# Kernel tuning notes

Hardware: AMD Instinct MI355X
Metric: run time of the kernel (lower is better)

## Reference

```python
import jax, jax.numpy as jnp
import numpy as np

B, I, O = 2048, 512, 512

def setup_inputs() -> dict:
    key = jax.random.key(0)
    kx, kw, ks = jax.random.split(key, 3)
    x = jax.random.uniform(kx, (B, I), dtype=jnp.float32)
    # shift weight logits so sigmoid(w) ~ 0.02: keeps the length-I product
    # of implication factors away from underflow (sparse conjunction)
    w_logits = jax.random.normal(kw, (I, O), dtype=jnp.float32) - 4.0
    s_logits = jax.random.normal(ks, (I, O), dtype=jnp.float32)
    return {"x": x, "w_logits": w_logits, "s_logits": s_logits}

def reference(x, w_logits, s_logits):
    # FuzzyParam.value(): sigmoid of stored logits
    w = jax.nn.sigmoid(w_logits)   # (I, O)
    s = jax.nn.sigmoid(s_logits)   # (I, O)
    xi = x[:, :, None]             # (B, I, 1)
    # product fuzzy logic:
    #   bin_xnor(a, b) = a*b + (1-a)*(1-b)
    #   implies(a, b)  = 1 - a*(1 - b)
    #   conjoin        = prod along axis
    xnor = xi * s + (1.0 - xi) * (1.0 - s)      # (B, I, O)
    factors = 1.0 - w * (1.0 - xnor)            # (B, I, O)
    return jnp.prod(factors, axis=1)            # (B, O)
```

## Files before the change

### kernel.cpp

```cpp
#include <hip/hip_runtime.h>
#include <math.h>

#define B_DIM 2048
#define I_DIM 512
#define O_DIM 512

constexpr int LANES = 64;
constexpr int T_O   = 4;
constexpr int O_BLK = LANES * T_O;
constexpr int NW    = 8;
constexpr int R_BLK = 8;
constexpr int QPC   = (I_DIM / 4) / NW;

__global__ __launch_bounds__(256) void setup_kernel(
    const float* __restrict__ w_logits,
    const float* __restrict__ s_logits,
    float4* __restrict__ ab4)
{
    int t  = blockIdx.x * 256 + threadIdx.x;
    int o  = t & (O_DIM - 1);
    int k  = t >> 9;
    int i0 = 2 * k;

    float zw0 = w_logits[(i0 + 0) * O_DIM + o];
    float zs0 = s_logits[(i0 + 0) * O_DIM + o];
    float zw1 = w_logits[(i0 + 1) * O_DIM + o];
    float zs1 = s_logits[(i0 + 1) * O_DIM + o];

    float w0 = 1.0f / (1.0f + expf(-zw0));
    float s0 = 1.0f / (1.0f + expf(-zs0));
    float w1 = 1.0f / (1.0f + expf(-zw1));
    float s1 = 1.0f / (1.0f + expf(-zs1));

    float4 v;
    v.x = fmaf(-w0, s0, 1.0f);
    v.y = fmaf(-w1, s1, 1.0f);
    v.z = w0 * (2.0f * s0 - 1.0f);
    v.w = w1 * (2.0f * s1 - 1.0f);
    ab4[k * O_DIM + o] = v;
}

__global__ __launch_bounds__(512, 2) void fuzzy_main(
    const float* __restrict__ x,
    const float4* __restrict__ ab4,
    float* __restrict__ out)
{
    __shared__ __align__(16) unsigned char sh_raw[64 * 1024];
    float (*part)[R_BLK][O_BLK] =
        reinterpret_cast<float(*)[R_BLK][O_BLK]>(sh_raw);

    const int lane  = threadIdx.x;
    const int y     = __builtin_amdgcn_readfirstlane((int)threadIdx.y);
    const int tid   = y * LANES + lane;
    const int bid   = blockIdx.x;
    const int obase = (bid & 1) * O_BLK;
    const int b0    = (bid >> 1) * R_BLK;
    const int qbase = y * QPC;

    const float* xb = x + (size_t)b0 * I_DIM + qbase * 4;

    const float4* abp = ab4 + obase + lane;

    float4 cA0[T_O], cA1[T_O], cB0[T_O], cB1[T_O];
#pragma unroll
    for (int j = 0; j < T_O; ++j) {
        cA0[j] = abp[(size_t)(2 * qbase + 0) * O_DIM + 64 * j];
        cA1[j] = abp[(size_t)(2 * qbase + 1) * O_DIM + 64 * j];
        cB0[j] = abp[(size_t)(2 * qbase + 2) * O_DIM + 64 * j];
        cB1[j] = abp[(size_t)(2 * qbase + 3) * O_DIM + 64 * j];
    }

    float acc[R_BLK][T_O];
#pragma unroll
    for (int r = 0; r < R_BLK; ++r)
#pragma unroll
        for (int j = 0; j < T_O; ++j) acc[r][j] = 1.0f;

#pragma unroll 1
    for (int qq = 0; qq < QPC; qq += 2) {
        float4 xqA[R_BLK], xqB[R_BLK];
#pragma unroll
        for (int r = 0; r < R_BLK; ++r) {
            const float* xr = xb + r * I_DIM + qq * 4;
            xqA[r] = *(const float4*)(xr);
            xqB[r] = *(const float4*)(xr + 4);
        }
        {
            const int q = qbase + qq;
            float4 nA0[T_O], nA1[T_O];
#pragma unroll
            for (int j = 0; j < T_O; ++j) {
                nA0[j] = abp[(size_t)(2 * q + 4) * O_DIM + 64 * j];
                nA1[j] = abp[(size_t)(2 * q + 5) * O_DIM + 64 * j];
            }
#pragma unroll
            for (int r = 0; r < R_BLK; ++r) {
#pragma unroll
                for (int j = 0; j < T_O; ++j) {
                    float f0 = fmaf(cA0[j].z, xqA[r].x, cA0[j].x);
                    float f1 = fmaf(cA0[j].w, xqA[r].y, cA0[j].y);
                    float f2 = fmaf(cA1[j].z, xqA[r].z, cA1[j].x);
                    float f3 = fmaf(cA1[j].w, xqA[r].w, cA1[j].y);
                    acc[r][j] *= (f0 * f2) * (f1 * f3);
                }
            }
#pragma unroll
            for (int j = 0; j < T_O; ++j) { cA0[j] = nA0[j]; cA1[j] = nA1[j]; }
        }
        {
            const int q = qbase + qq + 1;
            float4 nB0[T_O], nB1[T_O];
#pragma unroll
            for (int j = 0; j < T_O; ++j) {
                nB0[j] = abp[(size_t)(2 * q + 4) * O_DIM + 64 * j];
                nB1[j] = abp[(size_t)(2 * q + 5) * O_DIM + 64 * j];
            }
#pragma unroll
            for (int r = 0; r < R_BLK; ++r) {
#pragma unroll
                for (int j = 0; j < T_O; ++j) {
                    float f0 = fmaf(cB0[j].z, xqB[r].x, cB0[j].x);
                    float f1 = fmaf(cB0[j].w, xqB[r].y, cB0[j].y);
                    float f2 = fmaf(cB1[j].z, xqB[r].z, cB1[j].x);
                    float f3 = fmaf(cB1[j].w, xqB[r].w, cB1[j].y);
                    acc[r][j] *= (f0 * f2) * (f1 * f3);
                }
            }
#pragma unroll
            for (int j = 0; j < T_O; ++j) { cB0[j] = nB0[j]; cB1[j] = nB1[j]; }
        }
    }

    if (y < 4) {
#pragma unroll
        for (int r = 0; r < R_BLK; ++r)
#pragma unroll
            for (int j = 0; j < T_O; ++j)
                part[y][r][64 * j + lane] = acc[r][j];
    }
    __syncthreads();
    if (y >= 4) {
#pragma unroll
        for (int r = 0; r < R_BLK; ++r)
#pragma unroll
            for (int j = 0; j < T_O; ++j)
                part[y - 4][r][64 * j + lane] *= acc[r][j];
    }
    __syncthreads();
#pragma unroll
    for (int p = 0; p < 4; ++p) {
        int idx = p * 512 + tid;
        int r = idx >> 8;
        int c = idx & (O_BLK - 1);
        float v = part[0][r][c] * part[1][r][c]
                * part[2][r][c] * part[3][r][c];
        out[(size_t)(b0 + r) * O_DIM + obase + c] = v;
    }
}

extern "C" void kernel_launch(void* const* d_in, const int* in_sizes, int n_in,
                              void* d_out, int out_size, void* d_ws, size_t ws_size,
                              hipStream_t stream) {
    const float* x        = (const float*)d_in[0];
    const float* w_logits = (const float*)d_in[1];
    const float* s_logits = (const float*)d_in[2];
    float* out = (float*)d_out;
    float4* ab4 = (float4*)d_ws;

    setup_kernel<<<dim3(512), dim3(256), 0, stream>>>(w_logits, s_logits, ab4);

    fuzzy_main<<<dim3(512), dim3(LANES, NW), 0, stream>>>(
        x, ab4, out);
}
```

Measured before the change: 89.53 us.

## Factor out per-column constant product so inner loop uses one FMA per term

Rewrites each factor a+b*x as a*(1+(b/a)*x). The product of the a terms over I is precomputed per output column in two small setup kernels and applied once at the end. The main loop now loads one float4 of ratios per four inputs instead of two, which halves coefficient traffic and register use while keeping the same FMA and multiply count. It adds an extra single-block kernel launch and relies on a being nonzero and the product not underflowing, which can shift numerical rounding.

```diff
diff --git a/kernel.cpp b/kernel.cpp
--- a/kernel.cpp
+++ b/kernel.cpp
@@ -12,37 +12,57 @@
 constexpr int R_BLK = 8;
 constexpr int QPC   = (I_DIM / 4) / NW;
 
-__global__ __launch_bounds__(256) void setup_kernel(
+#define APROD_OFF (1u << 20)
+#define PO_OFF    ((1u << 20) + (1u << 18))
+
+__global__ __launch_bounds__(256) void setup_c(
     const float* __restrict__ w_logits,
     const float* __restrict__ s_logits,
-    float4* __restrict__ ab4)
+    float4* __restrict__ cT,
+    float*  __restrict__ aprod)
 {
-    int t  = blockIdx.x * 256 + threadIdx.x;
-    int o  = t & (O_DIM - 1);
-    int k  = t >> 9;
-    int i0 = 2 * k;
+    int t = blockIdx.x * 256 + threadIdx.x;
+    int o = t & (O_DIM - 1);
+    int q = t >> 9;
 
-    float zw0 = w_logits[(i0 + 0) * O_DIM + o];
-    float zs0 = s_logits[(i0 + 0) * O_DIM + o];
-    float zw1 = w_logits[(i0 + 1) * O_DIM + o];
-    float zs1 = s_logits[(i0 + 1) * O_DIM + o];
+    float c[4], pa = 1.0f;
+#pragma unroll
+    for (int u = 0; u < 4; ++u) {
+        int i = 4 * q + u;
+        float zw = w_logits[(size_t)i * O_DIM + o];
+        float zs = s_logits[(size_t)i * O_DIM + o];
+        float w = 1.0f / (1.0f + expf(-zw));
+        float s = 1.0f / (1.0f + expf(-zs));
+        float a = fmaf(-w, s, 1.0f);
+        float b = w * (2.0f * s - 1.0f);
+        c[u] = b / a;
+        pa *= a;
+    }
+    float4 v; v.x = c[0]; v.y = c[1]; v.z = c[2]; v.w = c[3];
+    cT[(size_t)q * O_DIM + o] = v;
+    aprod[(size_t)q * O_DIM + o] = pa;
+}
 
-    float w0 = 1.0f / (1.0f + expf(-zw0));
-    float s0 = 1.0f / (1.0f + expf(-zs0));
-    float w1 = 1.0f / (1.0f + expf(-zw1));
-    float s1 = 1.0f / (1.0f + expf(-zs1));
-
-    float4 v;
-    v.x = fmaf(-w0, s0, 1.0f);
-    v.y = fmaf(-w1, s1, 1.0f);
-    v.z = w0 * (2.0f * s0 - 1.0f);
-    v.w = w1 * (2.0f * s1 - 1.0f);
-    ab4[k * O_DIM + o] = v;
+__global__ __launch_bounds__(512) void setup_p(
+    const float* __restrict__ aprod,
+    float* __restrict__ pO)
+{
+    int o = threadIdx.x;
+    float p0 = 1.0f, p1 = 1.0f, p2 = 1.0f, p3 = 1.0f;
+#pragma unroll 8
+    for (int q = 0; q < 128; q += 4) {
+        p0 *= aprod[(size_t)(q + 0) * O_DIM + o];
+        p1 *= aprod[(size_t)(q + 1) * O_DIM + o];
+        p2 *= aprod[(size_t)(q + 2) * O_DIM + o];
+        p3 *= aprod[(size_t)(q + 3) * O_DIM + o];
+    }
+    pO[o] = (p0 * p1) * (p2 * p3);
 }
 
 __global__ __launch_bounds__(512, 2) void fuzzy_main(
     const float* __restrict__ x,
-    const float4* __restrict__ ab4,
+    const float4* __restrict__ cT,
+    const float* __restrict__ pO,
     float* __restrict__ out)
 {
     __shared__ __align__(16) unsigned char sh_raw[64 * 1024];
@@ -59,15 +79,13 @@
 
     const float* xb = x + (size_t)b0 * I_DIM + qbase * 4;
 
-    const float4* abp = ab4 + obase + lane;
+    const float4* cp = cT + obase + lane;
 
-    float4 cA0[T_O], cA1[T_O], cB0[T_O], cB1[T_O];
+    float4 cA[T_O], cB[T_O];
 #pragma unroll
     for (int j = 0; j < T_O; ++j) {
-        cA0[j] = abp[(size_t)(2 * qbase + 0) * O_DIM + 64 * j];
-        cA1[j] = abp[(size_t)(2 * qbase + 1) * O_DIM + 64 * j];
-        cB0[j] = abp[(size_t)(2 * qbase + 2) * O_DIM + 64 * j];
-        cB1[j] = abp[(size_t)(2 * qbase + 3) * O_DIM + 64 * j];
+        cA[j] = cp[(size_t)(qbase + 0) * O_DIM + 64 * j];
+        cB[j] = cp[(size_t)(qbase + 1) * O_DIM + 64 * j];
     }
 
     float acc[R_BLK][T_O];
@@ -87,47 +105,43 @@
         }
         {
             const int q = qbase + qq;
-            float4 nA0[T_O], nA1[T_O];
+            float4 nA[T_O];
 #pragma unroll
-            for (int j = 0; j < T_O; ++j) {
-                nA0[j] = abp[(size_t)(2 * q + 4) * O_DIM + 64 * j];
-                nA1[j] = abp[(size_t)(2 * q + 5) * O_DIM + 64 * j];
-            }
+            for (int j = 0; j < T_O; ++j)
+                nA[j] = cp[(size_t)(q + 2) * O_DIM + 64 * j];
 #pragma unroll
             for (int r = 0; r < R_BLK; ++r) {
 #pragma unroll
                 for (int j = 0; j < T_O; ++j) {
-                    float f0 = fmaf(cA0[j].z, xqA[r].x, cA0[j].x);
-                    float f1 = fmaf(cA0[j].w, xqA[r].y, cA0[j].y);
-                    float f2 = fmaf(cA1[j].z, xqA[r].z, cA1[j].x);
-                    float f3 = fmaf(cA1[j].w, xqA[r].w, cA1[j].y);
-                    acc[r][j] *= (f0 * f2) * (f1 * f3);
+                    float f0 = fmaf(cA[j].x, xqA[r].x, 1.0f);
+                    float f1 = fmaf(cA[j].y, xqA[r].y, 1.0f);
+                    float f2 = fmaf(cA[j].z, xqA[r].z, 1.0f);
+                    float f3 = fmaf(cA[j].w, xqA[r].w, 1.0f);
+                    acc[r][j] *= (f0 * f1) * (f2 * f3);
                 }
             }
 #pragma unroll
-            for (int j = 0; j < T_O; ++j) { cA0[j] = nA0[j]; cA1[j] = nA1[j]; }
+            for (int j = 0; j < T_O; ++j) cA[j] = nA[j];
         }
         {
             const int q = qbase + qq + 1;
-            float4 nB0[T_O], nB1[T_O];
+            float4 nB[T_O];
 #pragma unroll
-            for (int j = 0; j < T_O; ++j) {
-                nB0[j] = abp[(size_t)(2 * q + 4) * O_DIM + 64 * j];
-                nB1[j] = abp[(size_t)(2 * q + 5) * O_DIM + 64 * j];
-            }
+            for (int j = 0; j < T_O; ++j)
+                nB[j] = cp[(size_t)(q + 2) * O_DIM + 64 * j];
 #pragma unroll
             for (int r = 0; r < R_BLK; ++r) {
 #pragma unroll
                 for (int j = 0; j < T_O; ++j) {
-                    float f0 = fmaf(cB0[j].z, xqB[r].x, cB0[j].x);
-                    float f1 = fmaf(cB0[j].w, xqB[r].y, cB0[j].y);
-                    float f2 = fmaf(cB1[j].z, xqB[r].z, cB1[j].x);
-                    float f3 = fmaf(cB1[j].w, xqB[r].w, cB1[j].y);
-                    acc[r][j] *= (f0 * f2) * (f1 * f3);
+                    float f0 = fmaf(cB[j].x, xqB[r].x, 1.0f);
+                    float f1 = fmaf(cB[j].y, xqB[r].y, 1.0f);
+                    float f2 = fmaf(cB[j].z, xqB[r].z, 1.0f);
+                    float f3 = fmaf(cB[j].w, xqB[r].w, 1.0f);
+                    acc[r][j] *= (f0 * f1) * (f2 * f3);
                 }
             }
 #pragma unroll
-            for (int j = 0; j < T_O; ++j) { cB0[j] = nB0[j]; cB1[j] = nB1[j]; }
+            for (int j = 0; j < T_O; ++j) cB[j] = nB[j];
         }
     }
 
@@ -152,8 +166,9 @@
         int idx = p * 512 + tid;
         int r = idx >> 8;
         int c = idx & (O_BLK - 1);
-        float v = part[0][r][c] * part[1][r][c]
-                * part[2][r][c] * part[3][r][c];
+        float v = (part[0][r][c] * part[1][r][c])
+                * (part[2][r][c] * part[3][r][c]);
+        v *= pO[obase + c];
         out[(size_t)(b0 + r) * O_DIM + obase + c] = v;
     }
 }
@@ -165,10 +180,13 @@
     const float* w_logits = (const float*)d_in[1];
     const float* s_logits = (const float*)d_in[2];
     float* out = (float*)d_out;
-    float4* ab4 = (float4*)d_ws;
+    float4* cT    = (float4*)d_ws;
+    float*  aprod = (float*)((char*)d_ws + APROD_OFF);
+    float*  pOb   = (float*)((char*)d_ws + PO_OFF);
 
-    setup_kernel<<<dim3(512), dim3(256), 0, stream>>>(w_logits, s_logits, ab4);
+    setup_c<<<dim3(256), dim3(256), 0, stream>>>(w_logits, s_logits, cT, aprod);
+    setup_p<<<dim3(1), dim3(512), 0, stream>>>(aprod, pOb);
 
     fuzzy_main<<<dim3(512), dim3(LANES, NW), 0, stream>>>(
-        x, ab4, out);
+        x, cT, pOb, out);
 }
```

After: 88.40 us. Within noise of the previous version (-1.3%).
